# Performance work log

Hardware: AMD Instinct MI355X
Metric: run time of the kernel (lower is better)

Reference implementation:

```python
import jax, jax.numpy as jnp
import numpy as np

B, L, DM, DOUT, DST, DC, EXP, NB = 2, 4096, 256, 128, 16, 3, 2, 3
DI = EXP * DM          # 512 inner channels
DTR = (DM + 15) // 16  # dt_rank = 16


def setup_inputs() -> dict:
    nm = NB - 1
    ki = iter(jax.random.split(jax.random.key(0), 40))
    def rn(shape, s=0.02):
        return jax.random.normal(next(ki), shape, jnp.float32) * s
    A0 = jnp.log(jnp.tile(jnp.arange(1, DST + 1, dtype=jnp.float32), (DI, 1)))
    dtb0 = float(np.log(np.expm1(0.01)))  # softplus^-1(0.01)
    return {
        "x": jax.random.normal(next(ki), (B, L, DM), jnp.float32),
        "midW_in": rn((nm, 2 * DI, DM)),
        "midW_convw": rn((nm, DI, 1, DC), 0.1),
        "midW_convb": jnp.zeros((nm, DI), jnp.float32),
        "midW_x": rn((nm, DTR + 2 * DST, DI)),
        "midW_dtw": rn((nm, DI, DTR), 0.1),
        "midW_dtb": jnp.full((nm, DI), dtb0, jnp.float32),
        "midA_log": jnp.tile(A0, (nm, 1, 1)),
        "midD": jnp.ones((nm, DI), jnp.float32),
        "midW_out": rn((nm, DM, DI)),
        "midLNw": jnp.ones((nm, DM), jnp.float32),
        "midLNb": jnp.zeros((nm, DM), jnp.float32),
        "finW_in": rn((2 * DI, DM)),
        "finW_convw": rn((DI, 1, DC), 0.1),
        "finW_convb": jnp.zeros((DI,), jnp.float32),
        "finW_x": rn((DTR + 2 * DST, DI)),
        "finW_dtw": rn((DI, DTR), 0.1),
        "finW_dtb": jnp.full((DI,), dtb0, jnp.float32),
        "finA_log": A0,
        "finD": jnp.ones((DI,), jnp.float32),
        "finW_out": rn((DOUT, DI)),
        "finLNw": jnp.ones((DM,), jnp.float32),
        "finLNb": jnp.zeros((DM,), jnp.float32),
    }


def _layernorm(x, w, b):
    m = jnp.mean(x, -1, keepdims=True)
    v = jnp.var(x, -1, keepdims=True)
    return (x - m) * jax.lax.rsqrt(v + 1e-5) * w + b


def _selective_scan(dt, Bm, Cm, u, A):
    # dt,u: [B,L,DI]; Bm,Cm: [B,L,DST]; A: [DI,DST]
    def step(h, inp):
        dt_t, B_t, C_t, u_t = inp                      # [B,DI],[B,DST],[B,DST],[B,DI]
        dA = jnp.exp(dt_t[..., None] * A)              # [B,DI,DST]
        h = dA * h + (dt_t * u_t)[..., None] * B_t[:, None, :]
        return h, jnp.einsum('bdn,bn->bd', h, C_t)
    h0 = jnp.zeros((u.shape[0], A.shape[0], A.shape[1]), u.dtype)
    xs = (jnp.swapaxes(dt, 0, 1), jnp.swapaxes(Bm, 0, 1),
          jnp.swapaxes(Cm, 0, 1), jnp.swapaxes(u, 0, 1))
    _, ys = jax.lax.scan(step, h0, xs)
    return jnp.swapaxes(ys, 0, 1)


def _mamba(x, W_in, convw, convb, W_x, dtw, dtb, A_log, D, W_out):
    xz = jnp.einsum('bld,ed->ble', x, W_in)
    u, z = jnp.split(xz, 2, axis=-1)
    # causal depthwise conv over time
    uc = jax.lax.conv_general_dilated(jnp.swapaxes(u, 1, 2), convw, (1,), [(DC - 1, 0)],
                                      dimension_numbers=('NCH', 'OIH', 'NCH'),
                                      feature_group_count=DI)
    u = jax.nn.silu(jnp.swapaxes(uc, 1, 2) + convb)
    xdbl = jnp.einsum('bld,ed->ble', u, W_x)
    dt, Bm, Cm = xdbl[..., :DTR], xdbl[..., DTR:DTR + DST], xdbl[..., DTR + DST:]
    dt = jax.nn.softplus(jnp.einsum('blr,dr->bld', dt, dtw) + dtb)
    y = _selective_scan(dt, Bm, Cm, u, -jnp.exp(A_log))
    y = (y + u * D) * jax.nn.silu(z)
    return jnp.einsum('bld,od->blo', y, W_out)


def reference(x, midW_in, midW_convw, midW_convb, midW_x, midW_dtw, midW_dtb,
              midA_log, midD, midW_out, midLNw, midLNb,
              finW_in, finW_convw, finW_convb, finW_x, finW_dtw, finW_dtb,
              finA_log, finD, finW_out, finLNw, finLNb):
    res = None
    h = x
    for i in range(NB - 1):
        res = h if res is None else h + res
        hn = _layernorm(res, midLNw[i], midLNb[i])
        h = _mamba(hn, midW_in[i], midW_convw[i], midW_convb[i], midW_x[i],
                   midW_dtw[i], midW_dtb[i], midA_log[i], midD[i], midW_out[i])
    res = h if res is None else h + res
    hn = _layernorm(res, finLNw, finLNb)
    return _mamba(hn, finW_in, finW_convw, finW_convb, finW_x,
                  finW_dtw, finW_dtb, finA_log, finD, finW_out)
```

## Files before the change

kernel.cpp:

```cpp
#include <hip/hip_runtime.h>
#include <math.h>

#define Bsz   2
#define Lseq  4096
#define DMdim 256
#define DOUTd 128
#define DSTd  16
#define DId   512
#define DTRd  16
#define CS    32
#define NCh   128
#define NROWS (Bsz*Lseq)
#define N2    544

typedef short bf16x8 __attribute__((ext_vector_type(8)));
typedef float f32x4  __attribute__((ext_vector_type(4)));

#if __has_builtin(__builtin_amdgcn_exp2f)
#define EXP2F(x) __builtin_amdgcn_exp2f(x)
#else
#define EXP2F(x) __expf((x) * 0.69314718056f)
#endif
#define LOG2E 1.44269504f

__device__ __forceinline__ float siluf(float x) { return x / (1.f + __expf(-x)); }
__device__ __forceinline__ float softplusf(float x) {
  return fmaxf(x, 0.f) + log1pf(__expf(-fabsf(x)));
}
__device__ __forceinline__ unsigned short f2bf(float f) {
  union { float f; unsigned int u; } v; v.f = f;
  unsigned int r = v.u + 0x7fffu + ((v.u >> 16) & 1u);
  return (unsigned short)(r >> 16);
}
__device__ __forceinline__ float bf2f(unsigned short h) {
  union { unsigned int u; float f; } v; v.u = ((unsigned int)h) << 16;
  return v.f;
}

__global__ __launch_bounds__(256) void convert4_kernel(
    const float* __restrict__ s0, const float* __restrict__ s1,
    const float* __restrict__ s2, const float* __restrict__ s3,
    unsigned short* __restrict__ d0, unsigned short* __restrict__ d1,
    unsigned short* __restrict__ d2, unsigned short* __restrict__ d3,
    int n0, int n1, int n2, int n3)
{
  int i = blockIdx.x * 256 + threadIdx.x;
  int c0 = n0, c1 = c0 + n1, c2 = c1 + n2, c3 = c2 + n3;
  if (i >= c3) return;
  if      (i < c0) d0[i]      = f2bf(s0[i]);
  else if (i < c1) d1[i - c0] = f2bf(s1[i - c0]);
  else if (i < c2) d2[i - c1] = f2bf(s2[i - c1]);
  else             d3[i - c2] = f2bf(s3[i - c2]);
}

__global__ __launch_bounds__(256) void compose_kernel(
    const float* __restrict__ midW_x, const float* __restrict__ midW_dtw,
    const float* __restrict__ finW_x, const float* __restrict__ finW_dtw,
    unsigned short* __restrict__ W2)
{
  int lay = blockIdx.y;
  const float* Wx  = (lay < 2) ? midW_x  + (size_t)lay * 48 * DId : finW_x;
  const float* dtw = (lay < 2) ? midW_dtw + (size_t)lay * DId * 16 : finW_dtw;
  unsigned short* out = W2 + (size_t)lay * N2 * DId;
  int idx = blockIdx.x * 256 + threadIdx.x;
  if (idx >= N2 * DId) return;
  int n = idx >> 9, e = idx & (DId - 1);
  float v;
  if (n < 32) {
    v = Wx[(16 + n) * DId + e];
  } else {
    int d = n - 32;
    v = 0.f;
    #pragma unroll
    for (int r = 0; r < 16; r++) v = fmaf(dtw[d * 16 + r], Wx[r * DId + e], v);
  }
  out[idx] = f2bf(v);
}

__global__ __launch_bounds__(256) void resid_ln_kernel(
    const float* __restrict__ addsrc, float* __restrict__ res, unsigned short* __restrict__ hnb,
    const float* __restrict__ w, const float* __restrict__ b, int first)
{
  int row = blockIdx.x;
  int t = threadIdx.x;
  size_t o = (size_t)row * DMdim + t;
  float v = first ? addsrc[o] : (res[o] + addsrc[o]);
  res[o] = v;
  float s1 = v, s2 = v * v;
  #pragma unroll
  for (int m = 32; m >= 1; m >>= 1) {
    s1 += __shfl_xor(s1, m, 64);
    s2 += __shfl_xor(s2, m, 64);
  }
  __shared__ float w1[4], w2[4];
  int wid = t >> 6, ln = t & 63;
  if (ln == 0) { w1[wid] = s1; w2[wid] = s2; }
  __syncthreads();
  float S1 = w1[0] + w1[1] + w1[2] + w1[3];
  float S2 = w2[0] + w2[1] + w2[2] + w2[3];
  float mean = S1 * (1.f / DMdim);
  float var  = S2 * (1.f / DMdim) - mean * mean;
  float r = rsqrtf(var + 1e-5f);
  hnb[o] = f2bf((v - mean) * r * w[t] + b[t]);
}

__global__ __launch_bounds__(256) void gemm_bf_kernel(
    const unsigned short* __restrict__ A, const unsigned short* __restrict__ W,
    float* __restrict__ Cf0, float* __restrict__ Cf1,
    unsigned short* __restrict__ Cb0, unsigned short* __restrict__ Cb1,
    const float* __restrict__ bias2,
    int split, int N, int K, int mode)
{
  __shared__ unsigned short Abuf[4][128][8];
  __shared__ unsigned short Bbuf[4][64][8];
  int tid = threadIdx.x;
  int bm = blockIdx.x * 128;
  int bn = blockIdx.y * 64;
  int wid = tid >> 6, lane = tid & 63;
  int wm = wid >> 1, wn = wid & 1;
  int l15 = lane & 15, kh = lane >> 4;
  int r4 = tid >> 2;
  int c4 = tid & 3;
  f32x4 acc[4][2];
  #pragma unroll
  for (int i = 0; i < 4; i++)
    #pragma unroll
    for (int j = 0; j < 2; j++)
      #pragma unroll
      for (int r = 0; r < 4; r++) acc[i][j][r] = 0.f;

  for (int k0 = 0; k0 < K; k0 += 32) {
    const unsigned short* ga  = A + (size_t)(bm + r4) * K + k0 + c4 * 8;
    const unsigned short* ga2 = A + (size_t)(bm + 64 + r4) * K + k0 + c4 * 8;
    *(bf16x8*)&Abuf[c4][r4][0]      = *(const bf16x8*)ga;
    *(bf16x8*)&Abuf[c4][64 + r4][0] = *(const bf16x8*)ga2;
    int wr = bn + r4;
    bf16x8 wv;
    #pragma unroll
    for (int e = 0; e < 8; e++) wv[e] = 0;
    if (wr < N) wv = *(const bf16x8*)(W + (size_t)wr * K + k0 + c4 * 8);
    *(bf16x8*)&Bbuf[c4][r4][0] = wv;
    __syncthreads();
    bf16x8 af[4], bfr[2];
    #pragma unroll
    for (int i = 0; i < 4; i++)
      af[i] = *(const bf16x8*)&Abuf[kh][wm * 64 + i * 16 + l15][0];
    #pragma unroll
    for (int j = 0; j < 2; j++)
      bfr[j] = *(const bf16x8*)&Bbuf[kh][wn * 32 + j * 16 + l15][0];
    #pragma unroll
    for (int i = 0; i < 4; i++)
      #pragma unroll
      for (int j = 0; j < 2; j++)
        acc[i][j] = __builtin_amdgcn_mfma_f32_16x16x32_bf16(af[i], bfr[j], acc[i][j], 0, 0, 0);
    __syncthreads();
  }
  int mrow0 = bm + wm * 64 + (kh << 2);
  int ncol0 = bn + wn * 32 + l15;
  if (mode == 0) {
    int s0 = (split < N) ? split : N;
    int s1 = N - split;
    #pragma unroll
    for (int i = 0; i < 4; i++)
      #pragma unroll
      for (int j = 0; j < 2; j++) {
        int n = ncol0 + j * 16;
        if (n < N) {
          #pragma unroll
          for (int r = 0; r < 4; r++) {
            int m = mrow0 + i * 16 + r;
            if (n < split) Cf0[(size_t)m * s0 + n] = acc[i][j][r];
            else           Cf1[(size_t)m * s1 + (n - split)] = acc[i][j][r];
          }
        }
      }
  } else if (mode == 1) {
    #pragma unroll
    for (int i = 0; i < 4; i++)
      #pragma unroll
      for (int j = 0; j < 2; j++) {
        int n = ncol0 + j * 16;
        #pragma unroll
        for (int r = 0; r < 4; r++) {
          int m = mrow0 + i * 16 + r;
          if (n < split) Cb0[(size_t)m * DId + n] = f2bf(acc[i][j][r]);
          else           Cb1[(size_t)m * DId + (n - split)] = f2bf(acc[i][j][r]);
        }
      }
  } else {
    #pragma unroll
    for (int i = 0; i < 4; i++)
      #pragma unroll
      for (int j = 0; j < 2; j++) {
        int n = ncol0 + j * 16;
        if (n < N) {
          float bs = (n >= 32) ? bias2[n - 32] : 0.f;
          #pragma unroll
          for (int r = 0; r < 4; r++) {
            int m = mrow0 + i * 16 + r;
            if (n < 32) Cf0[(size_t)m * 32 + n] = acc[i][j][r];
            else        Cf1[(size_t)m * DId + (n - 32)] = softplusf(acc[i][j][r] + bs);
          }
        }
      }
  }
}

__global__ __launch_bounds__(256) void conv_silu_kernel(
    const unsigned short* __restrict__ ub, const float* __restrict__ cw,
    const float* __restrict__ cb, unsigned short* __restrict__ ucb)
{
  int idx = blockIdx.x * 256 + threadIdx.x;
  int d8 = (idx & 63) << 3;
  int bl = idx >> 6;
  int l  = bl & (Lseq - 1);
  bf16x8 u0 = *(const bf16x8*)(ub + (size_t)bl * DId + d8);
  bf16x8 u1, u2;
  #pragma unroll
  for (int e = 0; e < 8; e++) { u1[e] = 0; u2[e] = 0; }
  if (l >= 1) u1 = *(const bf16x8*)(ub + (size_t)(bl-1) * DId + d8);
  if (l >= 2) u2 = *(const bf16x8*)(ub + (size_t)(bl-2) * DId + d8);
  bf16x8 out;
  #pragma unroll
  for (int e = 0; e < 8; e++) {
    int d = d8 + e;
    float a = cb[d];
    a = fmaf(bf2f((unsigned short)u0[e]), cw[d*3+2], a);
    a = fmaf(bf2f((unsigned short)u1[e]), cw[d*3+1], a);
    a = fmaf(bf2f((unsigned short)u2[e]), cw[d*3+0], a);
    out[e] = (short)f2bf(siluf(a));
  }
  *(bf16x8*)(ucb + (size_t)bl * DId + d8) = out;
}

__global__ __launch_bounds__(256) void scan1_kernel(
    const float* __restrict__ dtf, const unsigned short* __restrict__ ucb,
    const float* __restrict__ xdbl, const float* __restrict__ A_log,
    float* __restrict__ hloc, float* __restrict__ Pst)
{
  int tid = threadIdx.x;
  int bx = blockIdx.x;
  int dh = bx & 1, c = (bx >> 1) & (NCh - 1), b = bx >> 8;
  int d = dh * 256 + tid;
  size_t base = (size_t)b * Lseq + (size_t)c * CS;
  float A2[16];
  #pragma unroll
  for (int q = 0; q < 4; q++) {
    float4 av = *(const float4*)(A_log + d * 16 + q * 4);
    A2[q*4+0] = -__expf(av.x) * LOG2E;
    A2[q*4+1] = -__expf(av.y) * LOG2E;
    A2[q*4+2] = -__expf(av.z) * LOG2E;
    A2[q*4+3] = -__expf(av.w) * LOG2E;
  }
  float dtv[CS], uv[CS];
  const float* dp = dtf + base * DId + d;
  const unsigned short* up = ucb + base * DId + d;
  #pragma unroll
  for (int t = 0; t < CS; t++) {
    dtv[t] = dp[(size_t)t * DId];
    uv[t]  = bf2f(up[(size_t)t * DId]);
  }
  const float* Bc = xdbl + base * 32;
  float h[16];
  #pragma unroll
  for (int n = 0; n < 16; n++) h[n] = 0.f;
  float sdt = 0.f;
  #pragma unroll 4
  for (int t = 0; t < CS; t++) {
    float dt = dtv[t];
    float du = dt * uv[t];
    sdt += dt;
    #pragma unroll
    for (int q = 0; q < 4; q++) {
      float4 Bv = *(const float4*)(Bc + t * 32 + q * 4);
      h[q*4+0] = fmaf(EXP2F(dt * A2[q*4+0]), h[q*4+0], du * Bv.x);
      h[q*4+1] = fmaf(EXP2F(dt * A2[q*4+1]), h[q*4+1], du * Bv.y);
      h[q*4+2] = fmaf(EXP2F(dt * A2[q*4+2]), h[q*4+2], du * Bv.z);
      h[q*4+3] = fmaf(EXP2F(dt * A2[q*4+3]), h[q*4+3], du * Bv.w);
    }
  }
  size_t so = (((size_t)(b * NCh + c) * DId) + d) * 16;
  #pragma unroll
  for (int q = 0; q < 4; q++) {
    float4 hv, pv;
    hv.x = h[q*4+0]; hv.y = h[q*4+1]; hv.z = h[q*4+2]; hv.w = h[q*4+3];
    pv.x = EXP2F(sdt * A2[q*4+0]);
    pv.y = EXP2F(sdt * A2[q*4+1]);
    pv.z = EXP2F(sdt * A2[q*4+2]);
    pv.w = EXP2F(sdt * A2[q*4+3]);
    *(float4*)(hloc + so + q * 4) = hv;
    *(float4*)(Pst  + so + q * 4) = pv;
  }
}

__global__ __launch_bounds__(256) void scan2_kernel(
    const float* __restrict__ hloc, const float* __restrict__ Pst,
    float* __restrict__ Hinit)
{
  int idx = blockIdx.x * 256 + threadIdx.x;
  int dn = idx & (DId * DSTd - 1);
  int b  = idx >> 13;
  float H = 0.f;
  #pragma unroll 4
  for (int c = 0; c < NCh; c++) {
    size_t o = ((size_t)(b * NCh + c)) * (DId * DSTd) + dn;
    Hinit[o] = H;
    H = fmaf(Pst[o], H, hloc[o]);
  }
}

__global__ __launch_bounds__(256) void scan3_kernel(
    const float* __restrict__ dtf, const unsigned short* __restrict__ ucb,
    const float* __restrict__ xdbl, const unsigned short* __restrict__ zb,
    const float* __restrict__ A_log, const float* __restrict__ Dv,
    const float* __restrict__ Hinit, unsigned short* __restrict__ yb)
{
  int tid = threadIdx.x;
  int bx = blockIdx.x;
  int dh = bx & 1, c = (bx >> 1) & (NCh - 1), b = bx >> 8;
  int d = dh * 256 + tid;
  size_t base = (size_t)b * Lseq + (size_t)c * CS;
  float A2[16];
  #pragma unroll
  for (int q = 0; q < 4; q++) {
    float4 av = *(const float4*)(A_log + d * 16 + q * 4);
    A2[q*4+0] = -__expf(av.x) * LOG2E;
    A2[q*4+1] = -__expf(av.y) * LOG2E;
    A2[q*4+2] = -__expf(av.z) * LOG2E;
    A2[q*4+3] = -__expf(av.w) * LOG2E;
  }
  float dtv[CS], uv[CS], zv[CS];
  const float* dp = dtf + base * DId + d;
  const unsigned short* up = ucb + base * DId + d;
  const unsigned short* zp = zb + base * DId + d;
  #pragma unroll
  for (int t = 0; t < CS; t++) {
    dtv[t] = dp[(size_t)t * DId];
    uv[t]  = bf2f(up[(size_t)t * DId]);
    zv[t]  = bf2f(zp[(size_t)t * DId]);
  }
  const float* Bc = xdbl + base * 32;
  size_t so = (((size_t)(b * NCh + c) * DId) + d) * 16;
  float h[16];
  #pragma unroll
  for (int q = 0; q < 4; q++) {
    float4 hv = *(const float4*)(Hinit + so + q * 4);
    h[q*4+0] = hv.x; h[q*4+1] = hv.y; h[q*4+2] = hv.z; h[q*4+3] = hv.w;
  }
  float Dd = Dv[d];
  #pragma unroll 4
  for (int t = 0; t < CS; t++) {
    float dt = dtv[t];
    float u  = uv[t];
    float du = dt * u;
    float y = 0.f;
    #pragma unroll
    for (int q = 0; q < 4; q++) {
      float4 Bv = *(const float4*)(Bc + t * 32 + q * 4);
      float4 Cv = *(const float4*)(Bc + t * 32 + 16 + q * 4);
      h[q*4+0] = fmaf(EXP2F(dt * A2[q*4+0]), h[q*4+0], du * Bv.x);
      h[q*4+1] = fmaf(EXP2F(dt * A2[q*4+1]), h[q*4+1], du * Bv.y);
      h[q*4+2] = fmaf(EXP2F(dt * A2[q*4+2]), h[q*4+2], du * Bv.z);
      h[q*4+3] = fmaf(EXP2F(dt * A2[q*4+3]), h[q*4+3], du * Bv.w);
      y = fmaf(h[q*4+0], Cv.x, y);
      y = fmaf(h[q*4+1], Cv.y, y);
      y = fmaf(h[q*4+2], Cv.z, y);
      y = fmaf(h[q*4+3], Cv.w, y);
    }
    yb[(base + t) * DId + d] = f2bf((y + u * Dd) * siluf(zv[t]));
  }
}

extern "C" void kernel_launch(void* const* d_in, const int* in_sizes, int n_in,
                              void* d_out, int out_size, void* d_ws, size_t ws_size,
                              hipStream_t stream)
{
  const float* x          = (const float*)d_in[0];
  const float* midW_in    = (const float*)d_in[1];
  const float* midW_convw = (const float*)d_in[2];
  const float* midW_convb = (const float*)d_in[3];
  const float* midW_x     = (const float*)d_in[4];
  const float* midW_dtw   = (const float*)d_in[5];
  const float* midW_dtb   = (const float*)d_in[6];
  const float* midA_log   = (const float*)d_in[7];
  const float* midD       = (const float*)d_in[8];
  const float* midW_out   = (const float*)d_in[9];
  const float* midLNw     = (const float*)d_in[10];
  const float* midLNb     = (const float*)d_in[11];
  const float* finW_in    = (const float*)d_in[12];
  const float* finW_convw = (const float*)d_in[13];
  const float* finW_convb = (const float*)d_in[14];
  const float* finW_x     = (const float*)d_in[15];
  const float* finW_dtw   = (const float*)d_in[16];
  const float* finW_dtb   = (const float*)d_in[17];
  const float* finA_log   = (const float*)d_in[18];
  const float* finD       = (const float*)d_in[19];
  const float* finW_out   = (const float*)d_in[20];
  const float* finLNw     = (const float*)d_in[21];
  const float* finLNb     = (const float*)d_in[22];

  float* ws    = (float*)d_ws;
  float* res   = ws;
  float* xdbl  = res   + 2097152;
  float* hloc  = xdbl  + 262144;
  float* Pst   = hloc  + 2097152;
  float* Hinit = Pst   + 2097152;
  float* hbuf  = Hinit + 2097152;
  float* dtf   = hbuf  + 2097152;
  unsigned short* us = (unsigned short*)(dtf + 4194304);
  unsigned short* hnb   = us;
  unsigned short* ub    = hnb  + 2097152;
  unsigned short* zbuf  = ub   + 4194304;
  unsigned short* ucb   = zbuf + 4194304;
  unsigned short* yb    = ucb  + 4194304;
  unsigned short* wWin  = yb   + 4194304;
  unsigned short* wWout = wWin + 524288;
  unsigned short* wfWin = wWout+ 262144;
  unsigned short* wfWout= wfWin+ 262144;
  unsigned short* wW2   = wfWout + 65536;

  {
    int n0 = 524288, n1 = 262144, n2 = 262144, n3 = 65536;
    int tot = n0 + n1 + n2 + n3;
    convert4_kernel<<<(tot + 255) / 256, 256, 0, stream>>>(
        midW_in, midW_out, finW_in, finW_out,
        wWin, wWout, wfWin, wfWout, n0, n1, n2, n3);
    dim3 gc((N2 * DId + 255) / 256, 3);
    compose_kernel<<<gc, 256, 0, stream>>>(midW_x, midW_dtw, finW_x, finW_dtw, wW2);
  }

  for (int blk = 0; blk < 3; blk++) {
    const unsigned short *Winb, *W2b, *Woutb;
    const float *convw, *convb, *dtb, *Alog, *Dv, *lnw, *lnb;
    int Nout;
    if (blk < 2) {
      Winb  = wWin  + (size_t)blk * 2*DId*DMdim;
      W2b   = wW2   + (size_t)blk * N2*DId;
      Woutb = wWout + (size_t)blk * DMdim*DId;
      convw = midW_convw + (size_t)blk * DId*3;
      convb = midW_convb + (size_t)blk * DId;
      dtb   = midW_dtb   + (size_t)blk * DId;
      Alog  = midA_log   + (size_t)blk * DId*DSTd;
      Dv    = midD       + (size_t)blk * DId;
      lnw   = midLNw     + (size_t)blk * DMdim;
      lnb   = midLNb     + (size_t)blk * DMdim;
      Nout  = DMdim;
    } else {
      Winb = wfWin; W2b = wW2 + (size_t)2 * N2*DId; Woutb = wfWout;
      convw = finW_convw; convb = finW_convb;
      dtb = finW_dtb; Alog = finA_log; Dv = finD;
      lnw = finLNw; lnb = finLNb;
      Nout = DOUTd;
    }
    const float* addsrc = (blk == 0) ? x : hbuf;
    resid_ln_kernel<<<NROWS, 256, 0, stream>>>(addsrc, res, hnb, lnw, lnb, blk == 0 ? 1 : 0);

    dim3 g1(NROWS/128, (2*DId)/64);
    gemm_bf_kernel<<<g1, 256, 0, stream>>>(hnb, Winb, nullptr, nullptr, ub, zbuf,
                                           nullptr, DId, 2*DId, DMdim, 1);

    conv_silu_kernel<<<(NROWS*64)/256, 256, 0, stream>>>(ub, convw, convb, ucb);

    dim3 g2(NROWS/128, (N2 + 63)/64);
    gemm_bf_kernel<<<g2, 256, 0, stream>>>(ucb, W2b, xdbl, dtf, nullptr, nullptr,
                                           dtb, 32, N2, DId, 2);

    scan1_kernel<<<Bsz*NCh*2, 256, 0, stream>>>(dtf, ucb, xdbl, Alog, hloc, Pst);
    scan2_kernel<<<64, 256, 0, stream>>>(hloc, Pst, Hinit);
    scan3_kernel<<<Bsz*NCh*2, 256, 0, stream>>>(dtf, ucb, xdbl, zbuf, Alog, Dv, Hinit, yb);

    float* Cout = (blk == 2) ? (float*)d_out : hbuf;
    dim3 g3(NROWS/128, (Nout + 63)/64);
    gemm_bf_kernel<<<g3, 256, 0, stream>>>(yb, Woutb, Cout, Cout, nullptr, nullptr,
                                           nullptr, Nout, Nout, DId, 0);
  }
}
```

Measured before the change: 497.0 us.

## Widen bf16 GEMM tile to 128x128 and load tiles directly into LDS

The shared bf16 MFMA GEMM now computes a 128x128 output tile per block instead of 128x64, so each wave holds 4x4 accumulators and each A tile loaded into LDS is reused across twice as many columns. Global-to-LDS staging uses the global_load_lds builtin with 16-byte transfers, which skips the round trip through registers. Out-of-range weight rows are clamped instead of zero-filled. The new row-major LDS layout with 64-byte row stride may cause bank conflicts on the fragment reads, and the larger tile halves the number of blocks and raises register pressure.

```diff
diff --git a/kernel.cpp b/kernel.cpp
--- a/kernel.cpp
+++ b/kernel.cpp
@@ -35,6 +35,12 @@
 __device__ __forceinline__ float bf2f(unsigned short h) {
   union { unsigned int u; float f; } v; v.u = ((unsigned int)h) << 16;
   return v.f;
+}
+
+__device__ __forceinline__ void gl2lds16(const void* g, void* l) {
+  __builtin_amdgcn_global_load_lds(
+      (const __attribute__((address_space(1))) void*)g,
+      (__attribute__((address_space(3))) void*)l, 16, 0, 0);
 }
 
 __global__ __launch_bounds__(256) void convert4_kernel(
@@ -111,74 +117,76 @@
     const float* __restrict__ bias2,
     int split, int N, int K, int mode)
 {
-  __shared__ unsigned short Abuf[4][128][8];
-  __shared__ unsigned short Bbuf[4][64][8];
+  __shared__ unsigned short As[128 * 32];
+  __shared__ unsigned short Bs[128 * 32];
   int tid = threadIdx.x;
-  int bm = blockIdx.x * 128;
-  int bn = blockIdx.y * 64;
   int wid = tid >> 6, lane = tid & 63;
   int wm = wid >> 1, wn = wid & 1;
   int l15 = lane & 15, kh = lane >> 4;
-  int r4 = tid >> 2;
-  int c4 = tid & 3;
-  f32x4 acc[4][2];
+  int bm = blockIdx.x * 128;
+  int bn = blockIdx.y * 128;
+
+  int srow = wid * 16 + (lane >> 2);
+  int schk = (lane & 3) * 8;
+  const unsigned short* gA0 = A + (size_t)(bm + srow) * K + schk;
+  const unsigned short* gA1 = A + (size_t)(bm + 64 + srow) * K + schk;
+  int wr0 = bn + srow;       if (wr0 >= N) wr0 = N - 1;
+  int wr1 = bn + 64 + srow;  if (wr1 >= N) wr1 = N - 1;
+  const unsigned short* gB0 = W + (size_t)wr0 * K + schk;
+  const unsigned short* gB1 = W + (size_t)wr1 * K + schk;
+  unsigned short* lA0 = As + wid * 512;
+  unsigned short* lA1 = As + 2048 + wid * 512;
+  unsigned short* lB0 = Bs + wid * 512;
+  unsigned short* lB1 = Bs + 2048 + wid * 512;
+
+  f32x4 acc[4][4];
   #pragma unroll
   for (int i = 0; i < 4; i++)
     #pragma unroll
-    for (int j = 0; j < 2; j++)
+    for (int j = 0; j < 4; j++)
       #pragma unroll
       for (int r = 0; r < 4; r++) acc[i][j][r] = 0.f;
 
   for (int k0 = 0; k0 < K; k0 += 32) {
-    const unsigned short* ga  = A + (size_t)(bm + r4) * K + k0 + c4 * 8;
-    const unsigned short* ga2 = A + (size_t)(bm + 64 + r4) * K + k0 + c4 * 8;
-    *(bf16x8*)&Abuf[c4][r4][0]      = *(const bf16x8*)ga;
-    *(bf16x8*)&Abuf[c4][64 + r4][0] = *(const bf16x8*)ga2;
-    int wr = bn + r4;
-    bf16x8 wv;
-    #pragma unroll
-    for (int e = 0; e < 8; e++) wv[e] = 0;
-    if (wr < N) wv = *(const bf16x8*)(W + (size_t)wr * K + k0 + c4 * 8);
-    *(bf16x8*)&Bbuf[c4][r4][0] = wv;
+    gl2lds16(gA0 + k0, lA0);
+    gl2lds16(gA1 + k0, lA1);
+    gl2lds16(gB0 + k0, lB0);
+    gl2lds16(gB1 + k0, lB1);
     __syncthreads();
-    bf16x8 af[4], bfr[2];
+    bf16x8 af[4], bfr[4];
     #pragma unroll
     for (int i = 0; i < 4; i++)
-      af[i] = *(const bf16x8*)&Abuf[kh][wm * 64 + i * 16 + l15][0];
-    #pragma unroll
-    for (int j = 0; j < 2; j++)
-      bfr[j] = *(const bf16x8*)&Bbuf[kh][wn * 32 + j * 16 + l15][0];
+      af[i] = *(const bf16x8*)(As + (wm * 64 + i * 16 + l15) * 32 + kh * 8);
+    #pragma unroll
+    for (int j = 0; j < 4; j++)
+      bfr[j] = *(const bf16x8*)(Bs + (wn * 64 + j * 16 + l15) * 32 + kh * 8);
     #pragma unroll
     for (int i = 0; i < 4; i++)
       #pragma unroll
-      for (int j = 0; j < 2; j++)
+      for (int j = 0; j < 4; j++)
         acc[i][j] = __builtin_amdgcn_mfma_f32_16x16x32_bf16(af[i], bfr[j], acc[i][j], 0, 0, 0);
     __syncthreads();
   }
+
   int mrow0 = bm + wm * 64 + (kh << 2);
-  int ncol0 = bn + wn * 32 + l15;
+  int ncol0 = bn + wn * 64 + l15;
   if (mode == 0) {
-    int s0 = (split < N) ? split : N;
-    int s1 = N - split;
     #pragma unroll
     for (int i = 0; i < 4; i++)
       #pragma unroll
-      for (int j = 0; j < 2; j++) {
+      for (int j = 0; j < 4; j++) {
         int n = ncol0 + j * 16;
         if (n < N) {
           #pragma unroll
-          for (int r = 0; r < 4; r++) {
-            int m = mrow0 + i * 16 + r;
-            if (n < split) Cf0[(size_t)m * s0 + n] = acc[i][j][r];
-            else           Cf1[(size_t)m * s1 + (n - split)] = acc[i][j][r];
-          }
+          for (int r = 0; r < 4; r++)
+            Cf0[(size_t)(mrow0 + i * 16 + r) * N + n] = acc[i][j][r];
         }
       }
   } else if (mode == 1) {
     #pragma unroll
     for (int i = 0; i < 4; i++)
       #pragma unroll
-      for (int j = 0; j < 2; j++) {
+      for (int j = 0; j < 4; j++) {
         int n = ncol0 + j * 16;
         #pragma unroll
         for (int r = 0; r < 4; r++) {
@@ -191,7 +199,7 @@
     #pragma unroll
     for (int i = 0; i < 4; i++)
       #pragma unroll
-      for (int j = 0; j < 2; j++) {
+      for (int j = 0; j < 4; j++) {
         int n = ncol0 + j * 16;
         if (n < N) {
           float bs = (n >= 32) ? bias2[n - 32] : 0.f;
@@ -455,13 +463,13 @@
     const float* addsrc = (blk == 0) ? x : hbuf;
     resid_ln_kernel<<<NROWS, 256, 0, stream>>>(addsrc, res, hnb, lnw, lnb, blk == 0 ? 1 : 0);
 
-    dim3 g1(NROWS/128, (2*DId)/64);
+    dim3 g1(NROWS/128, (2*DId)/128);
     gemm_bf_kernel<<<g1, 256, 0, stream>>>(hnb, Winb, nullptr, nullptr, ub, zbuf,
                                            nullptr, DId, 2*DId, DMdim, 1);
 
     conv_silu_kernel<<<(NROWS*64)/256, 256, 0, stream>>>(ub, convw, convb, ucb);
 
-    dim3 g2(NROWS/128, (N2 + 63)/64);
+    dim3 g2(NROWS/128, (N2 + 127)/128);
     gemm_bf_kernel<<<g2, 256, 0, stream>>>(ucb, W2b, xdbl, dtf, nullptr, nullptr,
                                            dtb, 32, N2, DId, 2);
 
@@ -470,8 +478,8 @@
     scan3_kernel<<<Bsz*NCh*2, 256, 0, stream>>>(dtf, ucb, xdbl, zbuf, Alog, Dv, Hinit, yb);
 
     float* Cout = (blk == 2) ? (float*)d_out : hbuf;
-    dim3 g3(NROWS/128, (Nout + 63)/64);
-    gemm_bf_kernel<<<g3, 256, 0, stream>>>(yb, Woutb, Cout, Cout, nullptr, nullptr,
+    dim3 g3(NROWS/128, (Nout + 127)/128);
+    gemm_bf_kernel<<<g3, 256, 0, stream>>>(yb, Woutb, Cout, nullptr, nullptr, nullptr,
                                            nullptr, Nout, Nout, DId, 0);
   }
 }
```

Result: slower. 516.6 us (+4.0%).
